# Performance work log

Measured on AMD Instinct MI355X. Metric: run time of the kernel, lower is better.

Reference implementation:

```python
import jax, jax.numpy as jnp
import numpy as np


def setup_inputs() -> dict:
    key = jax.random.key(0)
    kq, kk, kv = jax.random.split(key, 3)
    B, T, D = 8, 4096, 64
    q = jax.random.normal(kq, (B, T, D), dtype=jnp.float32)
    k = jax.random.normal(kk, (B, T, D), dtype=jnp.float32)
    v = jax.random.normal(kv, (B, T, D), dtype=jnp.float32)
    return {"q": q, "k": k, "v": v}


def reference(q, k, v):
    # q,k,v: [b, t, d]
    b, t_q, d = q.shape
    t_k = k.shape[1]
    scale = 1.0 / jnp.sqrt(jnp.asarray(d, dtype=q.dtype))
    qk = jnp.einsum('bqd,bkd->bqk', q, k) * scale  # [b, t_q, t_k]
    # causal mask: positions t2 > t1 set to -inf (replaces the Python double-loop)
    causal_mask = jnp.arange(t_k)[None, :] > jnp.arange(t_q)[:, None]  # [t_q, t_k]
    qk = jnp.where(causal_mask[None, :, :], -jnp.inf, qk)
    attn = jax.nn.softmax(qk, axis=-1)
    return jnp.einsum('bqk,bkd->bqd', attn, v)
```

## Files before the change

kernel.cpp:

```cpp
#include <hip/hip_runtime.h>

namespace {

constexpr float QSC = 0.18033688f;

typedef short bf16x8 __attribute__((ext_vector_type(8)));
typedef float f32x4 __attribute__((ext_vector_type(4)));

typedef __attribute__((address_space(3))) unsigned int lds_u32;
typedef __attribute__((address_space(1))) const unsigned int gbl_u32;

__device__ inline float exp2x(float x) { return __builtin_amdgcn_exp2f(x); }

__device__ inline unsigned int pack2(float a, float b) {
  unsigned int ua = __builtin_bit_cast(unsigned int, a);
  unsigned int ub = __builtin_bit_cast(unsigned int, b);
  ua = (ua + 0x8000u) >> 16;
  ub = (ub + 0x8000u) & 0xFFFF0000u;
  return ua | ub;
}

__device__ inline unsigned int cvtpk(float a, float b) {
  unsigned int r;
  asm("v_cvt_pk_bf16_f32 %0, %1, %2" : "=v"(r) : "v"(a), "v"(b));
  return r;
}

__device__ inline void gl_lds16(const unsigned short* g, unsigned short* l) {
  __builtin_amdgcn_global_load_lds((gbl_u32*)g, (lds_u32*)l, 16, 0, 0);
}

__device__ inline bf16x8 ld16(const unsigned short* p) {
  uint4 u = *(const uint4*)p;
  return __builtin_bit_cast(bf16x8, u);
}

__device__ inline void pswap32(unsigned int& a, unsigned int& b) {
  asm volatile("v_permlane32_swap_b32 %0, %1" : "+v"(a), "+v"(b));
}
__device__ inline void pswap16(unsigned int& a, unsigned int& b) {
  asm volatile("v_permlane16_swap_b32 %0, %1" : "+v"(a), "+v"(b));
}

__global__ __launch_bounds__(256) void prep(const float* __restrict__ K,
                                            const float* __restrict__ V,
                                            unsigned short* __restrict__ Kbf,
                                            unsigned short* __restrict__ Vtb) {
  __shared__ float Vl[64 * 65];
  const int bid = blockIdx.x;
  const int b = bid & 7, kt = bid >> 3;
  const int tid = threadIdx.x;
  const float4* Ks4 = (const float4*)(K + ((size_t)b * 4096 + kt * 64) * 64);
  const float4* Vs4 = (const float4*)(V + ((size_t)b * 4096 + kt * 64) * 64);
  #pragma unroll
  for (int i = 0; i < 4; ++i) {
    int idx = tid + 256 * i;
    int row = idx >> 4, c4 = idx & 15;
    float4 t = Ks4[idx];
    *(uint2*)&Kbf[((size_t)b * 4096 + kt * 64 + row) * 64 + c4 * 4] =
        make_uint2(pack2(t.x, t.y), pack2(t.z, t.w));
    float4 tv = Vs4[idx];
    float* d = &Vl[row * 65 + c4 * 4];
    d[0] = tv.x; d[1] = tv.y; d[2] = tv.z; d[3] = tv.w;
  }
  __syncthreads();
  #pragma unroll
  for (int i = 0; i < 4; ++i) {
    int idx = tid + 256 * i;
    int dd = idx >> 4, kc = idx & 15;
    float a  = Vl[(kc * 4 + 0) * 65 + dd];
    float b2 = Vl[(kc * 4 + 1) * 65 + dd];
    float c  = Vl[(kc * 4 + 2) * 65 + dd];
    float e  = Vl[(kc * 4 + 3) * 65 + dd];
    *(uint2*)&Vtb[((size_t)b * 64 + dd) * 4096 + kt * 64 + kc * 4] =
        make_uint2(pack2(a, b2), pack2(c, e));
  }
}

template <int NS>
__launch_bounds__(256, 4)
__global__ void fa_mfma(const float* __restrict__ Q,
                        float* __restrict__ O,
                        const unsigned short* __restrict__ Kbf,
                        const unsigned short* __restrict__ Vtb,
                        float* __restrict__ Opart,
                        float* __restrict__ lsum) {
  __shared__ __align__(16) unsigned short smem[16384];

  const int bid = blockIdx.x;
  const int b  = bid & 7;
  const int rr = bid >> 3;
  const int qt = 63 - rr / NS;
  const int s  = rr % NS;

  const int tid  = threadIdx.x;
  const int w    = tid >> 6;
  const int kh   = w & 1;
  const int qh   = w >> 1;
  const int lane = tid & 63;
  const int quad = lane >> 4;
  const int lc   = lane & 15;

  unsigned short* Kb0 = smem;
  unsigned short* Kb1 = smem + 4096;
  unsigned short* Vb0 = smem + 8192;
  unsigned short* Vb1 = smem + 12288;

  const unsigned short* Kt_g = Kbf + (size_t)b * 4096 * 64;
  const unsigned short* Vt_g = Vtb + (size_t)b * 64 * 4096;

  const int r0 = w * 16 + (lane >> 3);
  const int c0 = (lane & 7) ^ (r0 & 7);

  const int ph0 = (quad ^ (lc & 7)) * 8;
  const int ph1 = ((4 + quad) ^ (lc & 7)) * 8;
  const int phv = ((kh * 4 + quad) ^ (lc & 7)) * 8;

  const size_t tile_off = ((size_t)b * 4096 + (size_t)qt * 64) * 64;
  const float* Qb = Q + tile_off;

  const int nIter = (qt >= s) ? ((qt - s) / NS + 1) : 0;

  {
    const int kt0 = (s <= qt) ? s : qt;
    gl_lds16(Kt_g + (size_t)(kt0 * 64 + r0) * 64 + c0 * 8, Kb0 + w * 1024);
    gl_lds16(Kt_g + (size_t)(kt0 * 64 + r0 + 8) * 64 + c0 * 8, Kb0 + w * 1024 + 512);
    gl_lds16(Vt_g + (size_t)r0 * 4096 + kt0 * 64 + c0 * 8, Vb0 + w * 1024);
    gl_lds16(Vt_g + (size_t)(r0 + 8) * 4096 + kt0 * 64 + c0 * 8, Vb0 + w * 1024 + 512);
  }

  const unsigned short* gk0 = Kt_g + (size_t)((NS + s) * 64 + r0) * 64 + c0 * 8;
  const unsigned short* gk1 = gk0 + (size_t)8 * 64;
  const unsigned short* gv0 = Vt_g + (size_t)r0 * 4096 + (NS + s) * 64 + c0 * 8;
  const unsigned short* gv1 = gv0 + (size_t)8 * 4096;
  constexpr size_t K_STEP = (size_t)NS * 64 * 64;
  constexpr size_t V_STEP = (size_t)NS * 64;

  bf16x8 qf[2][2];
  #pragma unroll
  for (int tq = 0; tq < 2; ++tq) {
    const float* qrow = Qb + (qh * 32 + tq * 16 + lc) * 64 + quad * 8;
    #pragma unroll
    for (int ks = 0; ks < 2; ++ks) {
      float4 x = *(const float4*)(qrow + ks * 32);
      float4 y = *(const float4*)(qrow + ks * 32 + 4);
      uint4 u = make_uint4(pack2(x.x * QSC, x.y * QSC), pack2(x.z * QSC, x.w * QSC),
                           pack2(y.x * QSC, y.y * QSC), pack2(y.z * QSC, y.w * QSC));
      qf[tq][ks] = __builtin_bit_cast(bf16x8, u);
    }
  }

  float l4[2] = {0.0f, 0.0f};
  f32x4 o[2][4];
  #pragma unroll
  for (int tq = 0; tq < 2; ++tq)
    #pragma unroll
    for (int td = 0; td < 4; ++td) o[tq][td] = f32x4{0.f, 0.f, 0.f, 0.f};

  auto body = [&](const unsigned short* Kcur, const unsigned short* Vcur, bool diag) __attribute__((always_inline)) {
    bf16x8 kf[2][2];
    #pragma unroll
    for (int tk = 0; tk < 2; ++tk) {
      kf[tk][0] = ld16(&Kcur[(kh * 32 + tk * 16 + lc) * 64 + ph0]);
      kf[tk][1] = ld16(&Kcur[(kh * 32 + tk * 16 + lc) * 64 + ph1]);
    }
    f32x4 st[2][2];
    __builtin_amdgcn_s_setprio(1);
    #pragma unroll
    for (int tk = 0; tk < 2; ++tk)
      #pragma unroll
      for (int tq = 0; tq < 2; ++tq) {
        f32x4 c = {0.f, 0.f, 0.f, 0.f};
        c = __builtin_amdgcn_mfma_f32_16x16x32_bf16(kf[tk][0], qf[tq][0], c, 0, 0, 0);
        c = __builtin_amdgcn_mfma_f32_16x16x32_bf16(kf[tk][1], qf[tq][1], c, 0, 0, 0);
        st[tk][tq] = c;
      }
    __builtin_amdgcn_s_setprio(0);

    unsigned int pc[2][2][2];
    #pragma unroll
    for (int tk = 0; tk < 2; ++tk)
      #pragma unroll
      for (int tq = 0; tq < 2; ++tq) {
        float e[4];
        #pragma unroll
        for (int r = 0; r < 4; ++r) {
          float v = st[tk][tq][r];
          if (diag) {
            int key_l = kh * 32 + tk * 16 + quad * 4 + r;
            int q_l   = qh * 32 + tq * 16 + lc;
            if (key_l > q_l) v = -1e30f;
          }
          e[r] = exp2x(v);
        }
        l4[tq] += (e[0] + e[1]) + (e[2] + e[3]);
        pc[tk][tq][0] = cvtpk(e[0], e[1]);
        pc[tk][tq][1] = cvtpk(e[2], e[3]);
      }

    bf16x8 vf[4];
    #pragma unroll
    for (int td = 0; td < 4; ++td)
      vf[td] = ld16(&Vcur[(td * 16 + lc) * 64 + phv]);
    __builtin_amdgcn_s_setprio(1);
    #pragma unroll
    for (int tq = 0; tq < 2; ++tq) {
      unsigned int x0 = pc[0][tq][0], y0 = pc[1][tq][0];
      unsigned int x1 = pc[0][tq][1], y1 = pc[1][tq][1];
      pswap32(x0, y0); pswap16(x0, y0);
      pswap32(x1, y1); pswap16(x1, y1);
      bf16x8 a = __builtin_bit_cast(bf16x8, make_uint4(x0, x1, y0, y1));
      #pragma unroll
      for (int td = 0; td < 4; ++td)
        o[tq][td] = __builtin_amdgcn_mfma_f32_16x16x32_bf16(a, vf[td], o[tq][td], 0, 0, 0);
    }
    __builtin_amdgcn_s_setprio(0);
  };

  for (int i = 0; i + 1 < nIter; ++i) {
    const unsigned short* Kcur = (i & 1) ? Kb1 : Kb0;
    const unsigned short* Vcur = (i & 1) ? Vb1 : Vb0;
    unsigned short* Knxt = (i & 1) ? Kb0 : Kb1;
    unsigned short* Vnxt = (i & 1) ? Vb0 : Vb1;

    asm volatile("s_waitcnt vmcnt(0)" ::: "memory");
    __builtin_amdgcn_s_barrier();

    gl_lds16(gk0, Knxt + w * 1024);
    gl_lds16(gk1, Knxt + w * 1024 + 512);
    gl_lds16(gv0, Vnxt + w * 1024);
    gl_lds16(gv1, Vnxt + w * 1024 + 512);
    gk0 += K_STEP; gk1 += K_STEP; gv0 += V_STEP; gv1 += V_STEP;

    body(Kcur, Vcur, false);
  }

  if (nIter > 0) {
    const int il = nIter - 1;
    const unsigned short* Kcur = (il & 1) ? Kb1 : Kb0;
    const unsigned short* Vcur = (il & 1) ? Vb1 : Vb0;
    asm volatile("s_waitcnt vmcnt(0)" ::: "memory");
    __builtin_amdgcn_s_barrier();
    body(Kcur, Vcur, (NS * il + s) == qt);
  }

  __syncthreads();

  #pragma unroll
  for (int tq = 0; tq < 2; ++tq) {
    l4[tq] += __shfl_xor(l4[tq], 16);
    l4[tq] += __shfl_xor(l4[tq], 32);
  }

  constexpr int MS = 66;
  float* buf  = (float*)smem;
  float* lbuf = buf + 64 * MS;
  if (kh == 1) {
    #pragma unroll
    for (int tq = 0; tq < 2; ++tq) {
      #pragma unroll
      for (int r = 0; r < 4; ++r) {
        int row = qh * 32 + tq * 16 + quad * 4 + r;
        #pragma unroll
        for (int td = 0; td < 4; ++td)
          buf[row * MS + td * 16 + lc] = o[tq][td][r];
      }
      if (quad == 0) lbuf[qh * 32 + tq * 16 + lc] = l4[tq];
    }
  }
  __syncthreads();
  if (kh == 0) {
    #pragma unroll
    for (int tq = 0; tq < 2; ++tq) {
      l4[tq] += lbuf[qh * 32 + tq * 16 + lc];
      #pragma unroll
      for (int r = 0; r < 4; ++r) {
        int row = qh * 32 + tq * 16 + quad * 4 + r;
        #pragma unroll
        for (int td = 0; td < 4; ++td)
          o[tq][td][r] += buf[row * MS + td * 16 + lc];
      }
    }

    if constexpr (NS == 1) {
      float lv[2][4];
      #pragma unroll
      for (int tq = 0; tq < 2; ++tq) {
        float linv = 1.0f / l4[tq];
        #pragma unroll
        for (int r = 0; r < 4; ++r) lv[tq][r] = __shfl(linv, quad * 4 + r);
      }
      float* Ob = O + tile_off;
      #pragma unroll
      for (int tq = 0; tq < 2; ++tq)
        #pragma unroll
        for (int r = 0; r < 4; ++r) {
          int row = qh * 32 + tq * 16 + quad * 4 + r;
          #pragma unroll
          for (int td = 0; td < 4; ++td)
            Ob[row * 64 + td * 16 + lc] = o[tq][td][r] * lv[tq][r];
        }
    } else {
      float* Oslot = (s == 0) ? (O + tile_off)
                              : (Opart + (size_t)(s - 1) * 2097152 + tile_off);
      #pragma unroll
      for (int tq = 0; tq < 2; ++tq) {
        #pragma unroll
        for (int r = 0; r < 4; ++r) {
          int row = qh * 32 + tq * 16 + quad * 4 + r;
          #pragma unroll
          for (int td = 0; td < 4; ++td)
            Oslot[row * 64 + td * 16 + lc] = o[tq][td][r];
        }
        if (quad == 0)
          lsum[s * 32768 + b * 4096 + qt * 64 + qh * 32 + tq * 16 + lc] = l4[tq];
      }
    }
  }
}

template <int NS>
__global__ __launch_bounds__(256) void fa_merge(float* __restrict__ O,
                                               const float* __restrict__ Opart,
                                               const float* __restrict__ lsum) {
  const int b = blockIdx.x & 7;
  const int c = blockIdx.x >> 3;
  const int f = b * 262144 + c * 1024 + threadIdx.x * 4;
  const int row = f >> 6;
  float l = lsum[row];
  float4 acc = *(const float4*)&O[f];
  #pragma unroll
  for (int s2 = 1; s2 < NS; ++s2) {
    l += lsum[s2 * 32768 + row];
    float4 p = *(const float4*)&Opart[(size_t)(s2 - 1) * 2097152 + f];
    acc.x += p.x; acc.y += p.y; acc.z += p.z; acc.w += p.w;
  }
  const float linv = 1.0f / l;
  acc.x *= linv; acc.y *= linv; acc.z *= linv; acc.w *= linv;
  *(float4*)&O[f] = acc;
}

}

extern "C" void kernel_launch(void* const* d_in, const int* in_sizes, int n_in,
                              void* d_out, int out_size, void* d_ws, size_t ws_size,
                              hipStream_t stream) {
  const float* q = (const float*)d_in[0];
  const float* k = (const float*)d_in[1];
  const float* v = (const float*)d_in[2];
  float* out = (float*)d_out;

  unsigned short* Kbf = (unsigned short*)d_ws;
  unsigned short* Vtb = Kbf + (size_t)8 * 4096 * 64;
  float* Opart = (float*)(Vtb + (size_t)8 * 4096 * 64);
  auto need = [&](int ns) {
    return (size_t)16 * 1024 * 1024 / 2 +
           (size_t)(ns - 1) * 2097152 * 4 +
           (size_t)ns * 32768 * 4;
  };

  prep<<<dim3(512), dim3(256), 0, stream>>>(k, v, Kbf, Vtb);

  if (ws_size >= need(4)) {
    float* lsum = Opart + (size_t)3 * 2097152;
    fa_mfma<4><<<dim3(2048), dim3(256), 0, stream>>>(q, out, Kbf, Vtb, Opart, lsum);
    fa_merge<4><<<dim3(2048), dim3(256), 0, stream>>>(out, Opart, lsum);
  } else if (ws_size >= need(2)) {
    float* lsum = Opart + (size_t)1 * 2097152;
    fa_mfma<2><<<dim3(1024), dim3(256), 0, stream>>>(q, out, Kbf, Vtb, Opart, lsum);
    fa_merge<2><<<dim3(2048), dim3(256), 0, stream>>>(out, Opart, lsum);
  } else {
    fa_mfma<1><<<dim3(512), dim3(256), 0, stream>>>(q, out, Kbf, Vtb, nullptr, nullptr);
  }
}
```

Before: 109.9 us.

## Replace direct global-to-LDS loads with register-staged prefetch pipeline

Drops the global_load_lds async copies. Each K/V tile is now loaded into registers two iterations ahead and written to the alternate LDS buffer after the current tile's compute. The loop waits on lgkmcnt instead of vmcnt, so global load latency is meant to hide behind a full compute step. The cost is extra VGPRs for the staging registers, which may lower occupancy, and LDS store instructions issued by the compute waves.

```diff
diff --git a/kernel.cpp b/kernel.cpp
--- a/kernel.cpp
+++ b/kernel.cpp
@@ -6,9 +6,6 @@
 
 typedef short bf16x8 __attribute__((ext_vector_type(8)));
 typedef float f32x4 __attribute__((ext_vector_type(4)));
-
-typedef __attribute__((address_space(3))) unsigned int lds_u32;
-typedef __attribute__((address_space(1))) const unsigned int gbl_u32;
 
 __device__ inline float exp2x(float x) { return __builtin_amdgcn_exp2f(x); }
 
@@ -24,10 +21,6 @@
   unsigned int r;
   asm("v_cvt_pk_bf16_f32 %0, %1, %2" : "=v"(r) : "v"(a), "v"(b));
   return r;
-}
-
-__device__ inline void gl_lds16(const unsigned short* g, unsigned short* l) {
-  __builtin_amdgcn_global_load_lds((gbl_u32*)g, (lds_u32*)l, 16, 0, 0);
 }
 
 __device__ inline bf16x8 ld16(const unsigned short* p) {
@@ -111,6 +104,10 @@
 
   const int r0 = w * 16 + (lane >> 3);
   const int c0 = (lane & 7) ^ (r0 & 7);
+  const size_t koff = (size_t)r0 * 64 + (size_t)c0 * 8;
+  const size_t voff = (size_t)r0 * 4096 + (size_t)c0 * 8;
+  const int lw0 = w * 1024 + lane * 8;
+  const int lw1 = lw0 + 512;
 
   const int ph0 = (quad ^ (lc & 7)) * 8;
   const int ph1 = ((4 + quad) ^ (lc & 7)) * 8;
@@ -121,20 +118,15 @@
 
   const int nIter = (qt >= s) ? ((qt - s) / NS + 1) : 0;
 
-  {
-    const int kt0 = (s <= qt) ? s : qt;
-    gl_lds16(Kt_g + (size_t)(kt0 * 64 + r0) * 64 + c0 * 8, Kb0 + w * 1024);
-    gl_lds16(Kt_g + (size_t)(kt0 * 64 + r0 + 8) * 64 + c0 * 8, Kb0 + w * 1024 + 512);
-    gl_lds16(Vt_g + (size_t)r0 * 4096 + kt0 * 64 + c0 * 8, Vb0 + w * 1024);
-    gl_lds16(Vt_g + (size_t)(r0 + 8) * 4096 + kt0 * 64 + c0 * 8, Vb0 + w * 1024 + 512);
-  }
-
-  const unsigned short* gk0 = Kt_g + (size_t)((NS + s) * 64 + r0) * 64 + c0 * 8;
-  const unsigned short* gk1 = gk0 + (size_t)8 * 64;
-  const unsigned short* gv0 = Vt_g + (size_t)r0 * 4096 + (NS + s) * 64 + c0 * 8;
-  const unsigned short* gv1 = gv0 + (size_t)8 * 4096;
-  constexpr size_t K_STEP = (size_t)NS * 64 * 64;
-  constexpr size_t V_STEP = (size_t)NS * 64;
+  uint4 sK0 = {}, sK1 = {}, sV0 = {}, sV1 = {};
+  if (nIter > 0) {
+    const unsigned short* gkp = Kt_g + (size_t)s * 4096 + koff;
+    sK0 = *(const uint4*)gkp;
+    sK1 = *(const uint4*)(gkp + 8 * 64);
+    const unsigned short* gvp = Vt_g + (size_t)s * 64 + voff;
+    sV0 = *(const uint4*)gvp;
+    sV1 = *(const uint4*)(gvp + 8 * 4096);
+  }
 
   bf16x8 qf[2][2];
   #pragma unroll
@@ -147,6 +139,22 @@
       uint4 u = make_uint4(pack2(x.x * QSC, x.y * QSC), pack2(x.z * QSC, x.w * QSC),
                            pack2(y.x * QSC, y.y * QSC), pack2(y.z * QSC, y.w * QSC));
       qf[tq][ks] = __builtin_bit_cast(bf16x8, u);
+    }
+  }
+
+  if (nIter > 0) {
+    *(uint4*)&Kb0[lw0] = sK0;
+    *(uint4*)&Kb0[lw1] = sK1;
+    *(uint4*)&Vb0[lw0] = sV0;
+    *(uint4*)&Vb0[lw1] = sV1;
+    if (nIter > 1) {
+      const int kt1 = NS + s;
+      const unsigned short* gkp = Kt_g + (size_t)kt1 * 4096 + koff;
+      sK0 = *(const uint4*)gkp;
+      sK1 = *(const uint4*)(gkp + 8 * 64);
+      const unsigned short* gvp = Vt_g + (size_t)kt1 * 64 + voff;
+      sV0 = *(const uint4*)gvp;
+      sV1 = *(const uint4*)(gvp + 8 * 4096);
     }
   }
 
@@ -223,23 +231,32 @@
     unsigned short* Knxt = (i & 1) ? Kb0 : Kb1;
     unsigned short* Vnxt = (i & 1) ? Vb0 : Vb1;
 
-    asm volatile("s_waitcnt vmcnt(0)" ::: "memory");
+    asm volatile("s_waitcnt lgkmcnt(0)" ::: "memory");
     __builtin_amdgcn_s_barrier();
 
-    gl_lds16(gk0, Knxt + w * 1024);
-    gl_lds16(gk1, Knxt + w * 1024 + 512);
-    gl_lds16(gv0, Vnxt + w * 1024);
-    gl_lds16(gv1, Vnxt + w * 1024 + 512);
-    gk0 += K_STEP; gk1 += K_STEP; gv0 += V_STEP; gv1 += V_STEP;
-
     body(Kcur, Vcur, false);
+
+    *(uint4*)&Knxt[lw0] = sK0;
+    *(uint4*)&Knxt[lw1] = sK1;
+    *(uint4*)&Vnxt[lw0] = sV0;
+    *(uint4*)&Vnxt[lw1] = sV1;
+
+    if (i + 2 < nIter) {
+      const int ktn = NS * (i + 2) + s;
+      const unsigned short* gkp = Kt_g + (size_t)ktn * 4096 + koff;
+      sK0 = *(const uint4*)gkp;
+      sK1 = *(const uint4*)(gkp + 8 * 64);
+      const unsigned short* gvp = Vt_g + (size_t)ktn * 64 + voff;
+      sV0 = *(const uint4*)gvp;
+      sV1 = *(const uint4*)(gvp + 8 * 4096);
+    }
   }
 
   if (nIter > 0) {
     const int il = nIter - 1;
     const unsigned short* Kcur = (il & 1) ? Kb1 : Kb0;
     const unsigned short* Vcur = (il & 1) ? Vb1 : Vb0;
-    asm volatile("s_waitcnt vmcnt(0)" ::: "memory");
+    asm volatile("s_waitcnt lgkmcnt(0)" ::: "memory");
     __builtin_amdgcn_s_barrier();
     body(Kcur, Vcur, (NS * il + s) == qt);
   }
```

Result: no change. 108.2 us (-1.6%).
